# Performance work log

Hardware: AMD Instinct MI355X
Metric: run time of the kernel (lower is better)

## Reference

```python
import jax, jax.numpy as jnp
import numpy as np

B, IN, OUT = 512, 4096, 11008


def setup_inputs() -> dict:
    key = jax.random.key(0)
    k_x, k_stored, k_sign, k_scale, k_bias = jax.random.split(key, 5)
    x = jax.random.normal(k_x, (B, IN), dtype=jnp.float32)
    # QINS encoding: stored uint8 magnitude in [1, 255], sign in {-1, +1}
    stored = jax.random.randint(k_stored, (OUT, IN), 1, 256, dtype=jnp.int32)
    sign = 2 * jax.random.randint(k_sign, (OUT, IN), 0, 2, dtype=jnp.int32) - 1
    # log-range from from_linear's fallback calibration: weights in [e^-10, e^0]
    log_min = jnp.asarray(-10.0, dtype=jnp.float32)
    log_max = jnp.asarray(0.0, dtype=jnp.float32)
    # per-channel calibration scale, clamped to [0.5, 2.0] in from_linear
    scale = jax.random.uniform(k_scale, (OUT,), dtype=jnp.float32, minval=0.5, maxval=2.0)
    bias = jax.random.normal(k_bias, (OUT,), dtype=jnp.float32) * 0.01
    return {"x": x, "stored": stored, "sign": sign, "log_min": log_min,
            "log_max": log_max, "scale": scale, "bias": bias}


def reference(x, stored, sign, log_min, log_max, scale, bias):
    # Reconstruct fp32 weight from log-scale uint8 encoding (QINS)
    normalized = (255.0 - stored.astype(jnp.float32)) / 254.0      # [OUT, IN]
    log_w = log_min + normalized * (log_max - log_min)
    weight = sign.astype(jnp.float32) * jnp.exp(log_w)             # [OUT, IN]
    # y = (x @ W^T + b) * scale   (per-output-channel scale)
    out = jnp.einsum('bi,oi->bo', x, weight) + bias
    return out * scale
```

## Files before the change

### kernel.cpp

```cpp
#include <hip/hip_runtime.h>
#include <hip/hip_bf16.h>

#define B_DIM   512
#define IN_DIM  4096
#define OUT_DIM 11008

typedef __bf16 bf16x4 __attribute__((ext_vector_type(4)));
typedef __bf16 bf16x8 __attribute__((ext_vector_type(8)));
typedef float  floatx4 __attribute__((ext_vector_type(4)));

__global__ __launch_bounds__(256) void conv_x_kernel(
    const float* __restrict__ x, __bf16* __restrict__ xb) {
  int idx = blockIdx.x * blockDim.x + threadIdx.x;
  float4 v = ((const float4*)x)[idx];
  bf16x4 o;
  o[0] = (__bf16)v.x; o[1] = (__bf16)v.y; o[2] = (__bf16)v.z; o[3] = (__bf16)v.w;
  ((bf16x4*)xb)[idx] = o;
}

__device__ __forceinline__ void gl_lds16(const void* g, void* l) {
  __builtin_amdgcn_global_load_lds(
      (const __attribute__((address_space(1))) void*)g,
      (__attribute__((address_space(3))) void*)l, 16, 0, 0);
}

__device__ __forceinline__ float dec1f(int s, int g, float lmin, float slope) {
  float e = __expf(fmaf((float)(255 - s), slope, lmin));
  return __uint_as_float(__float_as_uint(e) ^ ((unsigned)g & 0x80000000u));
}

__device__ __forceinline__ bf16x8 dec8(int4 sl, int4 sh, int4 gl, int4 gh,
                                       float lmin, float slope) {
  bf16x8 w;
  w[0] = (__bf16)dec1f(sl.x, gl.x, lmin, slope);
  w[1] = (__bf16)dec1f(sl.y, gl.y, lmin, slope);
  w[2] = (__bf16)dec1f(sl.z, gl.z, lmin, slope);
  w[3] = (__bf16)dec1f(sl.w, gl.w, lmin, slope);
  w[4] = (__bf16)dec1f(sh.x, gh.x, lmin, slope);
  w[5] = (__bf16)dec1f(sh.y, gh.y, lmin, slope);
  w[6] = (__bf16)dec1f(sh.z, gh.z, lmin, slope);
  w[7] = (__bf16)dec1f(sh.w, gh.w, lmin, slope);
  return w;
}

__global__ __launch_bounds__(256, 3) void fused_qins_gemm_kernel(
    const __bf16* __restrict__ A,
    const int* __restrict__ stored,
    const int* __restrict__ sign,
    const float* __restrict__ logmin, const float* __restrict__ logmax,
    const float* __restrict__ scale, const float* __restrict__ bias,
    float* __restrict__ out) {
  constexpr int K = IN_DIM, N = OUT_DIM;
  constexpr int BK = 64;
  constexpr int NT = K / BK;

  __shared__ __align__(16) __bf16 sA[2][128 * BK];
  __shared__ __align__(16) __bf16 sB[2][64 * BK];

  const int tid  = threadIdx.x;
  const int lane = tid & 63;
  const int wave = tid >> 6;
  const int wm   = (wave >> 1) * 64;
  const int wn   = (wave & 1) * 32;
  const int m16  = lane & 15;
  const int q    = lane >> 4;

  const int wg  = blockIdx.x;
  const int g   = (wg & 7) * 86 + (wg >> 3);
  const int bm0 = (g & 3) * 128;
  const int bn0 = (g >> 2) * 64;

  const float lmin  = logmin[0];
  const float slope = (logmax[0] - lmin) * (1.0f / 254.0f);

  const int arow = tid >> 3;
  const int achk = (tid & 7) ^ (arow & 7);
  const __bf16* gA = A + (size_t)(bm0 + arow) * K + achk * 8;

  const int brow = tid >> 2;
  const int bsub = tid & 3;
  const int* pS = stored + (size_t)(bn0 + brow) * K + bsub * 16;
  const int* pG = sign   + (size_t)(bn0 + brow) * K + bsub * 16;
  const int wOff0 = brow * BK + (((2 * bsub)     ^ (brow & 7)) * 8);
  const int wOff1 = brow * BK + (((2 * bsub + 1) ^ (brow & 7)) * 8);

  const int slotk0 = ((4 * 0 + q) ^ (m16 & 7)) * 8;
  const int slotk1 = ((4 * 1 + q) ^ (m16 & 7)) * 8;

  floatx4 acc[4][2] = {};

  int4 s0, s1, s2, s3, g0, g1, g2, g3;
  s0 = *(const int4*)(pS);      s1 = *(const int4*)(pS + 4);
  s2 = *(const int4*)(pS + 8);  s3 = *(const int4*)(pS + 12);
  g0 = *(const int4*)(pG);      g1 = *(const int4*)(pG + 4);
  g2 = *(const int4*)(pG + 8);  g3 = *(const int4*)(pG + 12);
  *(bf16x8*)&sB[0][wOff0] = dec8(s0, s1, g0, g1, lmin, slope);
  *(bf16x8*)&sB[0][wOff1] = dec8(s2, s3, g2, g3, lmin, slope);
#pragma unroll
  for (int j = 0; j < 4; ++j)
    gl_lds16(gA + (size_t)j * 32 * K, &sA[0][j * 2048 + tid * 8]);
  s0 = *(const int4*)(pS + BK);      s1 = *(const int4*)(pS + BK + 4);
  s2 = *(const int4*)(pS + BK + 8);  s3 = *(const int4*)(pS + BK + 12);
  g0 = *(const int4*)(pG + BK);      g1 = *(const int4*)(pG + BK + 4);
  g2 = *(const int4*)(pG + BK + 8);  g3 = *(const int4*)(pG + BK + 12);
  __syncthreads();

  for (int t = 0; t < NT; ++t) {
    const int c = t & 1;

    *(bf16x8*)&sB[c ^ 1][wOff0] = dec8(s0, s1, g0, g1, lmin, slope);
    *(bf16x8*)&sB[c ^ 1][wOff1] = dec8(s2, s3, g2, g3, lmin, slope);

    const int ktA = ((t + 1 < NT) ? (t + 1) : 0) * BK;
#pragma unroll
    for (int j = 0; j < 4; ++j)
      gl_lds16(gA + (size_t)j * 32 * K + ktA, &sA[c ^ 1][j * 2048 + tid * 8]);

    const int ktB = ((t + 2 < NT) ? (t + 2) : 0) * BK;
    s0 = *(const int4*)(pS + ktB);      s1 = *(const int4*)(pS + ktB + 4);
    s2 = *(const int4*)(pS + ktB + 8);  s3 = *(const int4*)(pS + ktB + 12);
    g0 = *(const int4*)(pG + ktB);      g1 = *(const int4*)(pG + ktB + 4);
    g2 = *(const int4*)(pG + ktB + 8);  g3 = *(const int4*)(pG + ktB + 12);

    bf16x8 afr[4][2], bfr[2][2];
#pragma unroll
    for (int mi = 0; mi < 4; ++mi) {
      const int rbase = (wm + mi * 16 + m16) * BK;
      afr[mi][0] = *(const bf16x8*)&sA[c][rbase + slotk0];
      afr[mi][1] = *(const bf16x8*)&sA[c][rbase + slotk1];
    }
#pragma unroll
    for (int ni = 0; ni < 2; ++ni) {
      const int rbase = (wn + ni * 16 + m16) * BK;
      bfr[ni][0] = *(const bf16x8*)&sB[c][rbase + slotk0];
      bfr[ni][1] = *(const bf16x8*)&sB[c][rbase + slotk1];
    }

#pragma unroll
    for (int kk = 0; kk < 2; ++kk)
#pragma unroll
      for (int mi = 0; mi < 4; ++mi)
#pragma unroll
        for (int ni = 0; ni < 2; ++ni)
          acc[mi][ni] = __builtin_amdgcn_mfma_f32_16x16x32_bf16(
              afr[mi][kk], bfr[ni][kk], acc[mi][ni], 0, 0, 0);

    __syncthreads();
  }

#pragma unroll
  for (int ni = 0; ni < 2; ++ni) {
    const int col = bn0 + wn + ni * 16 + m16;
    const float sc = scale[col];
    const float bb = bias[col] * sc;
#pragma unroll
    for (int mi = 0; mi < 4; ++mi) {
#pragma unroll
      for (int r = 0; r < 4; ++r) {
        const int row = bm0 + wm + mi * 16 + q * 4 + r;
        out[row * N + col] = acc[mi][ni][r] * sc + bb;
      }
    }
  }
}

extern "C" void kernel_launch(void* const* d_in, const int* in_sizes, int n_in,
                              void* d_out, int out_size, void* d_ws, size_t ws_size,
                              hipStream_t stream) {
  const float* x      = (const float*)d_in[0];
  const int*   stored = (const int*)d_in[1];
  const int*   sign   = (const int*)d_in[2];
  const float* logmin = (const float*)d_in[3];
  const float* logmax = (const float*)d_in[4];
  const float* scale  = (const float*)d_in[5];
  const float* bias   = (const float*)d_in[6];
  float* out = (float*)d_out;

  __bf16* wsX = (__bf16*)d_ws;

  conv_x_kernel<<<2048, 256, 0, stream>>>(x, wsX);
  fused_qins_gemm_kernel<<<688, 256, 0, stream>>>(
      wsX, stored, sign, logmin, logmax, scale, bias, out);
}
```

Measured before the change: 468.8 us.

## Use 128x128 tiles with split-K of two and a separate reduction kernel

The output tile grows from 128x64 to 128x128, which halves how many times each weight row is decoded and read across M-blocks. K is split in two halves so the grid stays at 688 workgroups, and BK shrinks to 32. Partial sums go to fp32 workspace buffers, and a new reduce kernel adds them and applies bias and scale. In exchange the kernel writes and re-reads about 45 MB of partials and adds a launch, and the larger accumulator raises register pressure.

```diff
diff --git a/kernel.cpp b/kernel.cpp
--- a/kernel.cpp
+++ b/kernel.cpp
@@ -4,6 +4,7 @@
 #define B_DIM   512
 #define IN_DIM  4096
 #define OUT_DIM 11008
+#define PB      (B_DIM * OUT_DIM)
 
 typedef __bf16 bf16x4 __attribute__((ext_vector_type(4)));
 typedef __bf16 bf16x8 __attribute__((ext_vector_type(8)));
@@ -48,61 +49,62 @@
     const int* __restrict__ stored,
     const int* __restrict__ sign,
     const float* __restrict__ logmin, const float* __restrict__ logmax,
-    const float* __restrict__ scale, const float* __restrict__ bias,
-    float* __restrict__ out) {
+    float* __restrict__ part) {
   constexpr int K = IN_DIM, N = OUT_DIM;
-  constexpr int BK = 64;
-  constexpr int NT = K / BK;
+  constexpr int BK = 32;
+  constexpr int NT = 2048 / BK;
 
   __shared__ __align__(16) __bf16 sA[2][128 * BK];
-  __shared__ __align__(16) __bf16 sB[2][64 * BK];
+  __shared__ __align__(16) __bf16 sB[2][128 * BK];
 
   const int tid  = threadIdx.x;
   const int lane = tid & 63;
   const int wave = tid >> 6;
   const int wm   = (wave >> 1) * 64;
-  const int wn   = (wave & 1) * 32;
+  const int wn   = (wave & 1) * 64;
   const int m16  = lane & 15;
   const int q    = lane >> 4;
 
   const int wg  = blockIdx.x;
   const int g   = (wg & 7) * 86 + (wg >> 3);
-  const int bm0 = (g & 3) * 128;
-  const int bn0 = (g >> 2) * 64;
+  const int kh  = g / 344;
+  const int rem = g % 344;
+  const int bm0 = (rem & 3) * 128;
+  const int bn0 = (rem >> 2) * 128;
+  const int kbase = kh * 2048;
 
   const float lmin  = logmin[0];
   const float slope = (logmax[0] - lmin) * (1.0f / 254.0f);
 
-  const int arow = tid >> 3;
-  const int achk = (tid & 7) ^ (arow & 7);
-  const __bf16* gA = A + (size_t)(bm0 + arow) * K + achk * 8;
+  const int arow = tid >> 2;
+  const int achk = (tid & 3) ^ (arow & 3);
+  const __bf16* gA0 = A + (size_t)(bm0 + arow) * K + kbase + achk * 8;
+  const __bf16* gA1 = gA0 + (size_t)64 * K;
 
-  const int brow = tid >> 2;
-  const int bsub = tid & 3;
-  const int* pS = stored + (size_t)(bn0 + brow) * K + bsub * 16;
-  const int* pG = sign   + (size_t)(bn0 + brow) * K + bsub * 16;
-  const int wOff0 = brow * BK + (((2 * bsub)     ^ (brow & 7)) * 8);
-  const int wOff1 = brow * BK + (((2 * bsub + 1) ^ (brow & 7)) * 8);
+  const int rB  = tid >> 1;
+  const int bq2 = (tid & 1) * 2;
+  const int* pS = stored + (size_t)(bn0 + rB) * K + kbase + bq2 * 8;
+  const int* pG = sign   + (size_t)(bn0 + rB) * K + kbase + bq2 * 8;
+  const int wOff0 = rB * BK + ((bq2       ^ (rB & 3)) * 8);
+  const int wOff1 = rB * BK + (((bq2 + 1) ^ (rB & 3)) * 8);
 
-  const int slotk0 = ((4 * 0 + q) ^ (m16 & 7)) * 8;
-  const int slotk1 = ((4 * 1 + q) ^ (m16 & 7)) * 8;
+  const int slotB = (q ^ (m16 & 3)) * 8;
 
-  floatx4 acc[4][2] = {};
+  floatx4 acc[4][4] = {};
 
   int4 s0, s1, s2, s3, g0, g1, g2, g3;
-  s0 = *(const int4*)(pS);      s1 = *(const int4*)(pS + 4);
-  s2 = *(const int4*)(pS + 8);  s3 = *(const int4*)(pS + 12);
-  g0 = *(const int4*)(pG);      g1 = *(const int4*)(pG + 4);
-  g2 = *(const int4*)(pG + 8);  g3 = *(const int4*)(pG + 12);
+  s0 = *(const int4*)(pS);     s1 = *(const int4*)(pS + 4);
+  s2 = *(const int4*)(pS + 8); s3 = *(const int4*)(pS + 12);
+  g0 = *(const int4*)(pG);     g1 = *(const int4*)(pG + 4);
+  g2 = *(const int4*)(pG + 8); g3 = *(const int4*)(pG + 12);
   *(bf16x8*)&sB[0][wOff0] = dec8(s0, s1, g0, g1, lmin, slope);
   *(bf16x8*)&sB[0][wOff1] = dec8(s2, s3, g2, g3, lmin, slope);
-#pragma unroll
-  for (int j = 0; j < 4; ++j)
-    gl_lds16(gA + (size_t)j * 32 * K, &sA[0][j * 2048 + tid * 8]);
-  s0 = *(const int4*)(pS + BK);      s1 = *(const int4*)(pS + BK + 4);
-  s2 = *(const int4*)(pS + BK + 8);  s3 = *(const int4*)(pS + BK + 12);
-  g0 = *(const int4*)(pG + BK);      g1 = *(const int4*)(pG + BK + 4);
-  g2 = *(const int4*)(pG + BK + 8);  g3 = *(const int4*)(pG + BK + 12);
+  gl_lds16(gA0, &sA[0][tid * 8]);
+  gl_lds16(gA1, &sA[0][2048 + tid * 8]);
+  s0 = *(const int4*)(pS + BK);     s1 = *(const int4*)(pS + BK + 4);
+  s2 = *(const int4*)(pS + BK + 8); s3 = *(const int4*)(pS + BK + 12);
+  g0 = *(const int4*)(pG + BK);     g1 = *(const int4*)(pG + BK + 4);
+  g2 = *(const int4*)(pG + BK + 8); g3 = *(const int4*)(pG + BK + 12);
   __syncthreads();
 
   for (int t = 0; t < NT; ++t) {
@@ -112,56 +114,63 @@
     *(bf16x8*)&sB[c ^ 1][wOff1] = dec8(s2, s3, g2, g3, lmin, slope);
 
     const int ktA = ((t + 1 < NT) ? (t + 1) : 0) * BK;
-#pragma unroll
-    for (int j = 0; j < 4; ++j)
-      gl_lds16(gA + (size_t)j * 32 * K + ktA, &sA[c ^ 1][j * 2048 + tid * 8]);
+    gl_lds16(gA0 + ktA, &sA[c ^ 1][tid * 8]);
+    gl_lds16(gA1 + ktA, &sA[c ^ 1][2048 + tid * 8]);
 
     const int ktB = ((t + 2 < NT) ? (t + 2) : 0) * BK;
-    s0 = *(const int4*)(pS + ktB);      s1 = *(const int4*)(pS + ktB + 4);
-    s2 = *(const int4*)(pS + ktB + 8);  s3 = *(const int4*)(pS + ktB + 12);
-    g0 = *(const int4*)(pG + ktB);      g1 = *(const int4*)(pG + ktB + 4);
-    g2 = *(const int4*)(pG + ktB + 8);  g3 = *(const int4*)(pG + ktB + 12);
+    s0 = *(const int4*)(pS + ktB);     s1 = *(const int4*)(pS + ktB + 4);
+    s2 = *(const int4*)(pS + ktB + 8); s3 = *(const int4*)(pS + ktB + 12);
+    g0 = *(const int4*)(pG + ktB);     g1 = *(const int4*)(pG + ktB + 4);
+    g2 = *(const int4*)(pG + ktB + 8); g3 = *(const int4*)(pG + ktB + 12);
 
-    bf16x8 afr[4][2], bfr[2][2];
+    bf16x8 afr[4], bfr[4];
 #pragma unroll
-    for (int mi = 0; mi < 4; ++mi) {
-      const int rbase = (wm + mi * 16 + m16) * BK;
-      afr[mi][0] = *(const bf16x8*)&sA[c][rbase + slotk0];
-      afr[mi][1] = *(const bf16x8*)&sA[c][rbase + slotk1];
-    }
+    for (int mi = 0; mi < 4; ++mi)
+      afr[mi] = *(const bf16x8*)&sA[c][(wm + mi * 16 + m16) * BK + slotB];
 #pragma unroll
-    for (int ni = 0; ni < 2; ++ni) {
-      const int rbase = (wn + ni * 16 + m16) * BK;
-      bfr[ni][0] = *(const bf16x8*)&sB[c][rbase + slotk0];
-      bfr[ni][1] = *(const bf16x8*)&sB[c][rbase + slotk1];
-    }
+    for (int ni = 0; ni < 4; ++ni)
+      bfr[ni] = *(const bf16x8*)&sB[c][(wn + ni * 16 + m16) * BK + slotB];
 
 #pragma unroll
-    for (int kk = 0; kk < 2; ++kk)
+    for (int mi = 0; mi < 4; ++mi)
 #pragma unroll
-      for (int mi = 0; mi < 4; ++mi)
-#pragma unroll
-        for (int ni = 0; ni < 2; ++ni)
-          acc[mi][ni] = __builtin_amdgcn_mfma_f32_16x16x32_bf16(
-              afr[mi][kk], bfr[ni][kk], acc[mi][ni], 0, 0, 0);
+      for (int ni = 0; ni < 4; ++ni)
+        acc[mi][ni] = __builtin_amdgcn_mfma_f32_16x16x32_bf16(
+            afr[mi], bfr[ni], acc[mi][ni], 0, 0, 0);
 
     __syncthreads();
   }
 
+  float* p = part + (size_t)kh * PB;
 #pragma unroll
-  for (int ni = 0; ni < 2; ++ni) {
+  for (int ni = 0; ni < 4; ++ni) {
     const int col = bn0 + wn + ni * 16 + m16;
-    const float sc = scale[col];
-    const float bb = bias[col] * sc;
 #pragma unroll
     for (int mi = 0; mi < 4; ++mi) {
 #pragma unroll
       for (int r = 0; r < 4; ++r) {
         const int row = bm0 + wm + mi * 16 + q * 4 + r;
-        out[row * N + col] = acc[mi][ni][r] * sc + bb;
+        p[(size_t)row * N + col] = acc[mi][ni][r];
       }
     }
   }
+}
+
+__global__ __launch_bounds__(256) void reduce_kernel(
+    const float* __restrict__ part, const float* __restrict__ scale,
+    const float* __restrict__ bias, float* __restrict__ out) {
+  const int i4  = blockIdx.x * blockDim.x + threadIdx.x;
+  const int col = (i4 % (OUT_DIM / 4)) * 4;
+  float4 a = ((const float4*)part)[i4];
+  float4 b = ((const float4*)(part + PB))[i4];
+  float4 sc = *(const float4*)(scale + col);
+  float4 bb = *(const float4*)(bias + col);
+  float4 o;
+  o.x = (a.x + b.x + bb.x) * sc.x;
+  o.y = (a.y + b.y + bb.y) * sc.y;
+  o.z = (a.z + b.z + bb.z) * sc.z;
+  o.w = (a.w + b.w + bb.w) * sc.w;
+  ((float4*)out)[i4] = o;
 }
 
 extern "C" void kernel_launch(void* const* d_in, const int* in_sizes, int n_in,
@@ -176,9 +185,11 @@
   const float* bias   = (const float*)d_in[6];
   float* out = (float*)d_out;
 
-  __bf16* wsX = (__bf16*)d_ws;
+  float*  wsP = (float*)d_ws;
+  __bf16* wsX = (__bf16*)(wsP + 2 * (size_t)PB);
 
   conv_x_kernel<<<2048, 256, 0, stream>>>(x, wsX);
   fused_qins_gemm_kernel<<<688, 256, 0, stream>>>(
-      wsX, stored, sign, logmin, logmax, scale, bias, out);
+      wsX, stored, sign, logmin, logmax, wsP);
+  reduce_kernel<<<PB / 4 / 256, 256, 0, stream>>>(wsP, scale, bias, out);
 }
```

New measurement: 479.5 us. +2.3%, slower.

## Split weight decode into separate pass and use plain bf16 GEMM

Applied to the files above, without the earlier changes.

Replaces the fused decode-in-GEMM kernel with a standalone kernel that decodes the int32 stored/sign weights once into a bf16 workspace. A plain GEMM then streams both operands into LDS with async global-to-LDS loads. This removes redundant reads of the large int32 weight arrays and the repeated exp decode across the M-blocks. In exchange it adds a write and re-read of an intermediate bf16 weight buffer plus an extra launch.

```diff
diff --git a/kernel.cpp b/kernel.cpp
--- a/kernel.cpp
+++ b/kernel.cpp
@@ -8,21 +8,6 @@
 typedef __bf16 bf16x4 __attribute__((ext_vector_type(4)));
 typedef __bf16 bf16x8 __attribute__((ext_vector_type(8)));
 typedef float  floatx4 __attribute__((ext_vector_type(4)));
-
-__global__ __launch_bounds__(256) void conv_x_kernel(
-    const float* __restrict__ x, __bf16* __restrict__ xb) {
-  int idx = blockIdx.x * blockDim.x + threadIdx.x;
-  float4 v = ((const float4*)x)[idx];
-  bf16x4 o;
-  o[0] = (__bf16)v.x; o[1] = (__bf16)v.y; o[2] = (__bf16)v.z; o[3] = (__bf16)v.w;
-  ((bf16x4*)xb)[idx] = o;
-}
-
-__device__ __forceinline__ void gl_lds16(const void* g, void* l) {
-  __builtin_amdgcn_global_load_lds(
-      (const __attribute__((address_space(1))) void*)g,
-      (__attribute__((address_space(3))) void*)l, 16, 0, 0);
-}
 
 __device__ __forceinline__ float dec1f(int s, int g, float lmin, float slope) {
   float e = __expf(fmaf((float)(255 - s), slope, lmin));
@@ -43,11 +28,41 @@
   return w;
 }
 
-__global__ __launch_bounds__(256, 3) void fused_qins_gemm_kernel(
+__global__ __launch_bounds__(256) void decode_w_kernel(
+    const int* __restrict__ stored, const int* __restrict__ sign,
+    const float* __restrict__ logmin, const float* __restrict__ logmax,
+    __bf16* __restrict__ w) {
+  const float lmin  = logmin[0];
+  const float slope = (logmax[0] - lmin) * (1.0f / 254.0f);
+  constexpr int nG = OUT_DIM * IN_DIM / 8;
+  const int step = gridDim.x * blockDim.x;
+  for (int i = blockIdx.x * blockDim.x + threadIdx.x; i < nG; i += step) {
+    int4 s0 = ((const int4*)stored)[2 * i];
+    int4 s1 = ((const int4*)stored)[2 * i + 1];
+    int4 g0 = ((const int4*)sign)[2 * i];
+    int4 g1 = ((const int4*)sign)[2 * i + 1];
+    ((bf16x8*)w)[i] = dec8(s0, s1, g0, g1, lmin, slope);
+  }
+}
+
+__global__ __launch_bounds__(256) void conv_x_kernel(
+    const float* __restrict__ x, __bf16* __restrict__ xb) {
+  int idx = blockIdx.x * blockDim.x + threadIdx.x;
+  float4 v = ((const float4*)x)[idx];
+  bf16x4 o;
+  o[0] = (__bf16)v.x; o[1] = (__bf16)v.y; o[2] = (__bf16)v.z; o[3] = (__bf16)v.w;
+  ((bf16x4*)xb)[idx] = o;
+}
+
+__device__ __forceinline__ void gl_lds16(const void* g, void* l) {
+  __builtin_amdgcn_global_load_lds(
+      (const __attribute__((address_space(1))) void*)g,
+      (__attribute__((address_space(3))) void*)l, 16, 0, 0);
+}
+
+__global__ __launch_bounds__(256, 3) void gemm_bt_kernel(
     const __bf16* __restrict__ A,
-    const int* __restrict__ stored,
-    const int* __restrict__ sign,
-    const float* __restrict__ logmin, const float* __restrict__ logmax,
+    const __bf16* __restrict__ Bw,
     const float* __restrict__ scale, const float* __restrict__ bias,
     float* __restrict__ out) {
   constexpr int K = IN_DIM, N = OUT_DIM;
@@ -70,57 +85,34 @@
   const int bm0 = (g & 3) * 128;
   const int bn0 = (g >> 2) * 64;
 
-  const float lmin  = logmin[0];
-  const float slope = (logmax[0] - lmin) * (1.0f / 254.0f);
-
   const int arow = tid >> 3;
   const int achk = (tid & 7) ^ (arow & 7);
   const __bf16* gA = A + (size_t)(bm0 + arow) * K + achk * 8;
 
-  const int brow = tid >> 2;
-  const int bsub = tid & 3;
-  const int* pS = stored + (size_t)(bn0 + brow) * K + bsub * 16;
-  const int* pG = sign   + (size_t)(bn0 + brow) * K + bsub * 16;
-  const int wOff0 = brow * BK + (((2 * bsub)     ^ (brow & 7)) * 8);
-  const int wOff1 = brow * BK + (((2 * bsub + 1) ^ (brow & 7)) * 8);
+  const __bf16* gB = Bw + (size_t)(bn0 + arow) * K + achk * 8;
 
   const int slotk0 = ((4 * 0 + q) ^ (m16 & 7)) * 8;
   const int slotk1 = ((4 * 1 + q) ^ (m16 & 7)) * 8;
 
   floatx4 acc[4][2] = {};
 
-  int4 s0, s1, s2, s3, g0, g1, g2, g3;
-  s0 = *(const int4*)(pS);      s1 = *(const int4*)(pS + 4);
-  s2 = *(const int4*)(pS + 8);  s3 = *(const int4*)(pS + 12);
-  g0 = *(const int4*)(pG);      g1 = *(const int4*)(pG + 4);
-  g2 = *(const int4*)(pG + 8);  g3 = *(const int4*)(pG + 12);
-  *(bf16x8*)&sB[0][wOff0] = dec8(s0, s1, g0, g1, lmin, slope);
-  *(bf16x8*)&sB[0][wOff1] = dec8(s2, s3, g2, g3, lmin, slope);
 #pragma unroll
   for (int j = 0; j < 4; ++j)
     gl_lds16(gA + (size_t)j * 32 * K, &sA[0][j * 2048 + tid * 8]);
-  s0 = *(const int4*)(pS + BK);      s1 = *(const int4*)(pS + BK + 4);
-  s2 = *(const int4*)(pS + BK + 8);  s3 = *(const int4*)(pS + BK + 12);
-  g0 = *(const int4*)(pG + BK);      g1 = *(const int4*)(pG + BK + 4);
-  g2 = *(const int4*)(pG + BK + 8);  g3 = *(const int4*)(pG + BK + 12);
+#pragma unroll
+  for (int j = 0; j < 2; ++j)
+    gl_lds16(gB + (size_t)j * 32 * K, &sB[0][j * 2048 + tid * 8]);
   __syncthreads();
 
   for (int t = 0; t < NT; ++t) {
     const int c = t & 1;
-
-    *(bf16x8*)&sB[c ^ 1][wOff0] = dec8(s0, s1, g0, g1, lmin, slope);
-    *(bf16x8*)&sB[c ^ 1][wOff1] = dec8(s2, s3, g2, g3, lmin, slope);
-
-    const int ktA = ((t + 1 < NT) ? (t + 1) : 0) * BK;
+    const int ktn = ((t + 1 < NT) ? (t + 1) : 0) * BK;
 #pragma unroll
     for (int j = 0; j < 4; ++j)
-      gl_lds16(gA + (size_t)j * 32 * K + ktA, &sA[c ^ 1][j * 2048 + tid * 8]);
-
-    const int ktB = ((t + 2 < NT) ? (t + 2) : 0) * BK;
-    s0 = *(const int4*)(pS + ktB);      s1 = *(const int4*)(pS + ktB + 4);
-    s2 = *(const int4*)(pS + ktB + 8);  s3 = *(const int4*)(pS + ktB + 12);
-    g0 = *(const int4*)(pG + ktB);      g1 = *(const int4*)(pG + ktB + 4);
-    g2 = *(const int4*)(pG + ktB + 8);  g3 = *(const int4*)(pG + ktB + 12);
+      gl_lds16(gA + (size_t)j * 32 * K + ktn, &sA[c ^ 1][j * 2048 + tid * 8]);
+#pragma unroll
+    for (int j = 0; j < 2; ++j)
+      gl_lds16(gB + (size_t)j * 32 * K + ktn, &sB[c ^ 1][j * 2048 + tid * 8]);
 
     bf16x8 afr[4][2], bfr[2][2];
 #pragma unroll
@@ -176,9 +168,10 @@
   const float* bias   = (const float*)d_in[6];
   float* out = (float*)d_out;
 
-  __bf16* wsX = (__bf16*)d_ws;
+  __bf16* wsW = (__bf16*)d_ws;
+  __bf16* wsX = wsW + (size_t)OUT_DIM * IN_DIM;
 
+  decode_w_kernel<<<2048, 256, 0, stream>>>(stored, sign, logmin, logmax, wsW);
   conv_x_kernel<<<2048, 256, 0, stream>>>(x, wsX);
-  fused_qins_gemm_kernel<<<688, 256, 0, stream>>>(
-      wsX, stored, sign, logmin, logmax, scale, bias, out);
+  gemm_bt_kernel<<<688, 256, 0, stream>>>(wsX, wsW, scale, bias, out);
 }
```

Measured after the change: 498.0 us. 1.06x slower.
